# Kernel tuning notes

Hardware: AMD Instinct MI355X
Metric: run time of the kernel (lower is better)

Reference implementation:

```python
import jax, jax.numpy as jnp
import numpy as np

# Synthetic kinematic tree: 1 root + C0 chains of L0 atoms (generation 0 scans,
# rooted at node 0) + C1 branches of L1 atoms rooted mid-chain (generation 1 scans).
C0, L0 = 2048, 768
C1, L1 = 2048, 256
N = 1 + C0 * L0 + C1 * L1  # 2_097_153 atoms (incl. virtual root)


def setup_inputs() -> dict:
    key = jax.random.key(0)
    dofs = jax.random.normal(key, (N, 9), dtype=jnp.float32)

    chain_starts = 1 + np.arange(C0, dtype=np.int64) * L0          # first atom of each chain
    gen0 = np.concatenate(
        [np.zeros((C0, 1), np.int64),
         chain_starts[:, None] + np.arange(L0)[None, :]], axis=1)    # [C0, L0+1], col0 = root

    branch_roots = chain_starts + L0 // 2                            # computed during gen 0
    boff = 1 + C0 * L0
    gen1 = np.concatenate(
        [branch_roots[:, None],
         boff + (np.arange(C1, dtype=np.int64) * L1)[:, None] + np.arange(L1)[None, :]],
        axis=1)                                                      # [C1, L1+1]

    doftype = np.full((N,), 2, np.int32)  # BOND
    doftype[0] = 0                        # ROOT
    doftype[chain_starts] = 1             # JUMP at each chain start

    # kintree.id[1:] -> coords index: a fixed permutation (irregular scatter)
    id_idx = np.random.default_rng(0).permutation(N - 1).astype(np.int32)

    return {
        "dofs": dofs,
        "doftype": jnp.asarray(doftype),
        "gen0_paths": jnp.asarray(gen0, dtype=jnp.int32),
        "gen1_paths": jnp.asarray(gen1, dtype=jnp.int32),
        "id_idx": jnp.asarray(id_idx),
    }


def _rx(a):
    c, s = jnp.cos(a), jnp.sin(a)
    o, z = jnp.ones_like(a), jnp.zeros_like(a)
    return jnp.stack([jnp.stack([o, z, z, z], -1),
                      jnp.stack([z, c, -s, z], -1),
                      jnp.stack([z, s, c, z], -1),
                      jnp.stack([z, z, z, o], -1)], -2)


def _ry(a):
    c, s = jnp.cos(a), jnp.sin(a)
    o, z = jnp.ones_like(a), jnp.zeros_like(a)
    return jnp.stack([jnp.stack([c, z, s, z], -1),
                      jnp.stack([z, o, z, z], -1),
                      jnp.stack([-s, z, c, z], -1),
                      jnp.stack([z, z, z, o], -1)], -2)


def _rz(a):
    c, s = jnp.cos(a), jnp.sin(a)
    o, z = jnp.ones_like(a), jnp.zeros_like(a)
    return jnp.stack([jnp.stack([c, -s, z, z], -1),
                      jnp.stack([s, c, z, z], -1),
                      jnp.stack([z, z, o, z], -1),
                      jnp.stack([z, z, z, o], -1)], -2)


def _trans(x, y, z):
    o, zr = jnp.ones_like(x), jnp.zeros_like(x)
    return jnp.stack([jnp.stack([o, zr, zr, x], -1),
                      jnp.stack([zr, o, zr, y], -1),
                      jnp.stack([zr, zr, o, z], -1),
                      jnp.stack([zr, zr, zr, o], -1)], -2)


def _local_hts(dofs, doftype):
    # BOND dofs: phi_p, theta, d, phi_c  (NeRF-style internal coordinates)
    phi_p, theta, d, phi_c = dofs[:, 0], dofs[:, 1], dofs[:, 2], dofs[:, 3]
    z = jnp.zeros_like(d)
    bond = _rx(phi_p) @ _rz(jnp.pi - theta) @ _trans(d, z, z) @ _rx(phi_c)
    # JUMP dofs: RBx,RBy,RBz, RBdel_(a,b,c), RB_(a,b,c)
    rot = lambda a, b, c: _rz(c) @ _ry(b) @ _rx(a)
    jump = (_trans(dofs[:, 0], dofs[:, 1], dofs[:, 2])
            @ rot(dofs[:, 3], dofs[:, 4], dofs[:, 5])
            @ rot(dofs[:, 6], dofs[:, 7], dofs[:, 8]))
    eye = jnp.broadcast_to(jnp.eye(4, dtype=dofs.dtype), bond.shape)
    dt = doftype[:, None, None]
    return jnp.where(dt == 1, jump, jnp.where(dt == 2, bond, eye))


def reference(dofs, doftype, gen0_paths, gen1_paths, id_idx):
    hts = _local_hts(dofs, doftype)  # [N, 4, 4] local HTs; root = identity
    # Generation-ordered segmented scan: within each generation, each scan path's
    # first node already holds its GLOBAL HT; compose child = parent @ local along
    # the path via an associative prefix-matmul, then scatter back.
    for paths in (gen0_paths, gen1_paths):
        seg = hts[paths]                                        # [S, Lp, 4, 4]
        scanned = jax.lax.associative_scan(jnp.matmul, seg, axis=1)
        hts = hts.at[paths].set(scanned)
    kincoords = hts[:, :3, 3]                                   # [N, 3]
    coords = jnp.zeros((N - 1, 3), dtype=dofs.dtype)
    coords = coords.at[id_idx].set(kincoords[1:])               # coords[id[1:]] = kincoords[1:]
    return coords
```

## Files before the change

### kernel.cpp

```cpp
#include <hip/hip_runtime.h>
#include <math.h>

#define NC0 2048
#define NL0 768
#define NL1 256
#define BOFF (1 + NC0 * NL0)

struct Aff { float f[12]; };

__device__ __forceinline__ Aff affIdentity() {
    Aff M;
    M.f[0]=1.f; M.f[1]=0.f; M.f[2]=0.f;
    M.f[3]=0.f; M.f[4]=1.f; M.f[5]=0.f;
    M.f[6]=0.f; M.f[7]=0.f; M.f[8]=1.f;
    M.f[9]=0.f; M.f[10]=0.f; M.f[11]=0.f;
    return M;
}

__device__ __forceinline__ Aff compose(const Aff& A, const Aff& B) {
    Aff C;
#pragma unroll
    for (int i = 0; i < 3; ++i) {
        const float a0 = A.f[i*3+0], a1 = A.f[i*3+1], a2 = A.f[i*3+2];
#pragma unroll
        for (int j = 0; j < 3; ++j)
            C.f[i*3+j] = a0*B.f[0*3+j] + a1*B.f[1*3+j] + a2*B.f[2*3+j];
        C.f[9+i] = a0*B.f[9] + a1*B.f[10] + a2*B.f[11] + A.f[9+i];
    }
    return C;
}

__device__ __forceinline__ void applyA(const Aff& A, float& x, float& y, float& z) {
    const float nx = A.f[0]*x + A.f[1]*y + A.f[2]*z + A.f[9];
    const float ny = A.f[3]*x + A.f[4]*y + A.f[5]*z + A.f[10];
    const float nz = A.f[6]*x + A.f[7]*y + A.f[8]*z + A.f[11];
    x = nx; y = ny; z = nz;
}

__device__ __forceinline__ Aff shflUpA(const Aff& A, int d) {
    Aff B;
#pragma unroll
    for (int k = 0; k < 12; ++k) B.f[k] = __shfl_up(A.f[k], d, 64);
    return B;
}

__device__ __forceinline__ void fsc(float a, float& s, float& c) {
    s = __sinf(a);
    c = __cosf(a);
}

__device__ __forceinline__ Aff bondHT(float phi_p, float theta, float dd, float phi_c) {
    float sp, cp, st, ct, sc, cc;
    fsc(phi_p, sp, cp);
    fsc(theta, st, ct);
    fsc(phi_c, sc, cc);
    const float ca = -ct, sa = st;
    const float r00 = ca,    r01 = -sa;
    const float r10 = cp*sa, r11 = cp*ca,  r12 = -sp;
    const float r20 = sp*sa, r21 = sp*ca,  r22 = cp;
    Aff M;
    M.f[0] = r00; M.f[1] = r01*cc;          M.f[2] = -r01*sc;
    M.f[3] = r10; M.f[4] = r11*cc + r12*sc; M.f[5] = -r11*sc + r12*cc;
    M.f[6] = r20; M.f[7] = r21*cc + r22*sc; M.f[8] = -r21*sc + r22*cc;
    M.f[9] = r00*dd; M.f[10] = r10*dd; M.f[11] = r20*dd;
    return M;
}

__device__ __forceinline__ void rot3(float a, float b, float c, float* R) {
    float sa, ca, sb, cb, sg, cg;
    fsc(a, sa, ca);
    fsc(b, sb, cb);
    fsc(c, sg, cg);
    R[0] = cb*cg; R[1] = sa*sb*cg - ca*sg; R[2] = ca*sb*cg + sa*sg;
    R[3] = cb*sg; R[4] = sa*sb*sg + ca*cg; R[5] = ca*sb*sg - sa*cg;
    R[6] = -sb;   R[7] = sa*cb;            R[8] = ca*cb;
}

__device__ __forceinline__ Aff jumpHT(float d0, float d1, float d2,
                                      float d3, float d4, float d5,
                                      float d6, float d7, float d8) {
    float R1[9], R2[9];
    rot3(d3, d4, d5, R1);
    rot3(d6, d7, d8, R2);
    Aff M;
#pragma unroll
    for (int i = 0; i < 3; ++i)
#pragma unroll
        for (int j = 0; j < 3; ++j)
            M.f[i*3+j] = R1[i*3+0]*R2[0*3+j] + R1[i*3+1]*R2[1*3+j] + R1[i*3+2]*R2[2*3+j];
    M.f[9] = d0; M.f[10] = d1; M.f[11] = d2;
    return M;
}

__device__ __forceinline__ void stA(float* sm, int i, const Aff& A) {
    float* p = sm + i * 12;
#pragma unroll
    for (int k = 0; k < 12; ++k) p[k] = A.f[k];
}
__device__ __forceinline__ Aff ldA(const float* sm, int i) {
    const float* p = sm + i * 12;
    Aff A;
#pragma unroll
    for (int k = 0; k < 12; ++k) A.f[k] = p[k];
    return A;
}

__global__ __launch_bounds__(256, 4)
void kin_kernel(const float* __restrict__ dofs,
                const int* __restrict__ id_idx,
                float* __restrict__ out) {
    __shared__ float wt0[4 * 12];
    __shared__ float wt1[4 * 12];
    __shared__ float rootSm[12];

    const int c    = blockIdx.x;
    const int t    = threadIdx.x;
    const int lane = t & 63;
    const int wave = t >> 6;

    const int pos = 3 * t;
    const int n0  = 1 + c * NL0 + pos;
    const float* db  = dofs + (size_t)n0 * 9;
    const float* dbb = dofs + (size_t)(BOFF + c * NL1 + t) * 9;

    const float a0 = db[0],  a1 = db[1],  a2 = db[2],  a3 = db[3];
    const float b0 = db[9],  b1 = db[10], b2 = db[11], b3 = db[12];
    const float c0 = db[18], c1 = db[19], c2 = db[20], c3 = db[21];
    const float e0 = dbb[0], e1 = dbb[1], e2 = dbb[2], e3 = dbb[3];

    const int obase = c * NL0 + pos;
    const int oi0 = id_idx[obase + 0];
    const int oi1 = id_idx[obase + 1];
    const int oi2 = id_idx[obase + 2];
    const int oib = id_idx[(BOFF - 1) + c * NL1 + t];

    Aff P1;
    if (t == 0) {
        const float j4 = db[4], j5 = db[5], j6 = db[6], j7 = db[7], j8 = db[8];
        P1 = jumpHT(a0, a1, a2, a3, j4, j5, j6, j7, j8);
    } else {
        P1 = bondHT(a0, a1, a2, a3);
    }
    const Aff P2 = compose(P1, bondHT(b0, b1, b2, b3));
    const Aff P3 = compose(P2, bondHT(c0, c1, c2, c3));
    Aff Sb = bondHT(e0, e1, e2, e3);

    Aff S = P3;
#pragma unroll
    for (int s = 1; s < 64; s <<= 1) {
        const Aff A = shflUpA(S, s);
        const Aff B = shflUpA(Sb, s);
        if (lane >= s) {
            S  = compose(A, S);
            Sb = compose(B, Sb);
        }
    }
    if (lane == 63) { stA(wt0, wave, S); stA(wt1, wave, Sb); }
    __syncthreads();

    Aff E = shflUpA(S, 1);
    Aff EW;
    if (wave == 0) {
        if (lane == 0) E = affIdentity();
        EW = E;
    } else {
        Aff W = ldA(wt0, 0);
        for (int w = 1; w < wave; ++w) W = compose(W, ldA(wt0, w));
        EW = (lane == 0) ? W : compose(W, E);
    }

    float x0 = P1.f[9], y0 = P1.f[10], z0 = P1.f[11]; applyA(EW, x0, y0, z0);
    float x1 = P2.f[9], y1 = P2.f[10], z1 = P2.f[11]; applyA(EW, x1, y1, z1);
    float x2 = P3.f[9], y2 = P3.f[10], z2 = P3.f[11]; applyA(EW, x2, y2, z2);

    if (t == 128) {
        const Aff G = compose(EW, P1);
        stA(rootSm, 0, G);
    }

    float vx = Sb.f[9], vy = Sb.f[10], vz = Sb.f[11];
    for (int w = wave - 1; w >= 0; --w) {
        const Aff Wb = ldA(wt1, w);
        applyA(Wb, vx, vy, vz);
    }
    __syncthreads();

    const Aff R = ldA(rootSm, 0);
    applyA(R, vx, vy, vz);

    float* o;
    o = out + (size_t)oi0 * 3; o[0] = x0; o[1] = y0; o[2] = z0;
    o = out + (size_t)oi1 * 3; o[0] = x1; o[1] = y1; o[2] = z1;
    o = out + (size_t)oi2 * 3; o[0] = x2; o[1] = y2; o[2] = z2;
    o = out + (size_t)oib * 3; o[0] = vx; o[1] = vy; o[2] = vz;
}

extern "C" void kernel_launch(void* const* d_in, const int* in_sizes, int n_in,
                              void* d_out, int out_size, void* d_ws, size_t ws_size,
                              hipStream_t stream) {
    const float* dofs   = (const float*)d_in[0];
    const int*   id_idx = (const int*)d_in[4];
    float*       out    = (float*)d_out;

    hipLaunchKernelGGL(kin_kernel, dim3(NC0), dim3(256), 0, stream,
                       dofs, id_idx, out);
}
```

Before: 163.1 us.

## Use one wave per chain with 12 atoms per thread and vectorized loads

```diff
diff --git a/kernel.cpp b/kernel.cpp
--- a/kernel.cpp
+++ b/kernel.cpp
@@ -28,13 +28,6 @@
         C.f[9+i] = a0*B.f[9] + a1*B.f[10] + a2*B.f[11] + A.f[9+i];
     }
     return C;
-}
-
-__device__ __forceinline__ void applyA(const Aff& A, float& x, float& y, float& z) {
-    const float nx = A.f[0]*x + A.f[1]*y + A.f[2]*z + A.f[9];
-    const float ny = A.f[3]*x + A.f[4]*y + A.f[5]*z + A.f[10];
-    const float nz = A.f[6]*x + A.f[7]*y + A.f[8]*z + A.f[11];
-    x = nx; y = ny; z = nz;
 }
 
 __device__ __forceinline__ Aff shflUpA(const Aff& A, int d) {
@@ -92,107 +85,117 @@
     return M;
 }
 
-__device__ __forceinline__ void stA(float* sm, int i, const Aff& A) {
-    float* p = sm + i * 12;
-#pragma unroll
-    for (int k = 0; k < 12; ++k) p[k] = A.f[k];
-}
-__device__ __forceinline__ Aff ldA(const float* sm, int i) {
-    const float* p = sm + i * 12;
-    Aff A;
-#pragma unroll
-    for (int k = 0; k < 12; ++k) A.f[k] = p[k];
-    return A;
-}
-
-__global__ __launch_bounds__(256, 4)
+__device__ __forceinline__ float f4c(const float4 v, int j) {
+    return j == 0 ? v.x : j == 1 ? v.y : j == 2 ? v.z : v.w;
+}
+__device__ __forceinline__ int i4c(const int4 v, int j) {
+    return j == 0 ? v.x : j == 1 ? v.y : j == 2 ? v.z : v.w;
+}
+
+#define GFA(m) f4c(ch[((m)+1)>>2], ((m)+1)&3)
+#define GFB(m) f4c(chb[((m)+1)>>2], ((m)+1)&3)
+
+__global__ __launch_bounds__(64)
 void kin_kernel(const float* __restrict__ dofs,
                 const int* __restrict__ id_idx,
                 float* __restrict__ out) {
-    __shared__ float wt0[4 * 12];
-    __shared__ float wt1[4 * 12];
-    __shared__ float rootSm[12];
-
-    const int c    = blockIdx.x;
-    const int t    = threadIdx.x;
-    const int lane = t & 63;
-    const int wave = t >> 6;
-
-    const int pos = 3 * t;
-    const int n0  = 1 + c * NL0 + pos;
-    const float* db  = dofs + (size_t)n0 * 9;
-    const float* dbb = dofs + (size_t)(BOFF + c * NL1 + t) * 9;
-
-    const float a0 = db[0],  a1 = db[1],  a2 = db[2],  a3 = db[3];
-    const float b0 = db[9],  b1 = db[10], b2 = db[11], b3 = db[12];
-    const float c0 = db[18], c1 = db[19], c2 = db[20], c3 = db[21];
-    const float e0 = dbb[0], e1 = dbb[1], e2 = dbb[2], e3 = dbb[3];
-
-    const int obase = c * NL0 + pos;
-    const int oi0 = id_idx[obase + 0];
-    const int oi1 = id_idx[obase + 1];
-    const int oi2 = id_idx[obase + 2];
-    const int oib = id_idx[(BOFF - 1) + c * NL1 + t];
-
-    Aff P1;
-    if (t == 0) {
-        const float j4 = db[4], j5 = db[5], j6 = db[6], j7 = db[7], j8 = db[8];
-        P1 = jumpHT(a0, a1, a2, a3, j4, j5, j6, j7, j8);
-    } else {
-        P1 = bondHT(a0, a1, a2, a3);
-    }
-    const Aff P2 = compose(P1, bondHT(b0, b1, b2, b3));
-    const Aff P3 = compose(P2, bondHT(c0, c1, c2, c3));
-    Aff Sb = bondHT(e0, e1, e2, e3);
-
-    Aff S = P3;
+    const int c = blockIdx.x;
+    const int t = threadIdx.x;
+
+    const int ib0 = c * NL0 + 12 * t;
+    const int4 i0 = *(const int4*)(id_idx + ib0 + 0);
+    const int4 i1 = *(const int4*)(id_idx + ib0 + 4);
+    const int4 i2 = *(const int4*)(id_idx + ib0 + 8);
+    const int4 ibv = *(const int4*)(id_idx + (BOFF - 1) + c * NL1 + 4 * t);
+
+    const float4* g4 = (const float4*)dofs;
+    const size_t f0  = (size_t)(1 + c * NL0 + 12 * t) * 9;
+    const size_t cb0 = (f0 - 1) >> 2;
+    float4 ch[26];
+    ch[0]  = g4[cb0 + 0];  ch[1]  = g4[cb0 + 1];  ch[2]  = g4[cb0 + 2];
+    ch[3]  = g4[cb0 + 3];  ch[4]  = g4[cb0 + 4];  ch[5]  = g4[cb0 + 5];
+    ch[7]  = g4[cb0 + 7];  ch[9]  = g4[cb0 + 9];  ch[10] = g4[cb0 + 10];
+    ch[11] = g4[cb0 + 11]; ch[12] = g4[cb0 + 12]; ch[13] = g4[cb0 + 13];
+    ch[14] = g4[cb0 + 14]; ch[16] = g4[cb0 + 16]; ch[18] = g4[cb0 + 18];
+    ch[19] = g4[cb0 + 19]; ch[20] = g4[cb0 + 20]; ch[21] = g4[cb0 + 21];
+    ch[22] = g4[cb0 + 22]; ch[23] = g4[cb0 + 23]; ch[25] = g4[cb0 + 25];
+
+    const size_t f1  = (size_t)(BOFF + c * NL1 + 4 * t) * 9;
+    const size_t cb1 = (f1 - 1) >> 2;
+    float4 chb[8];
+    chb[0] = g4[cb1 + 0]; chb[1] = g4[cb1 + 1]; chb[2] = g4[cb1 + 2];
+    chb[3] = g4[cb1 + 3]; chb[4] = g4[cb1 + 4]; chb[5] = g4[cb1 + 5];
+    chb[7] = g4[cb1 + 7];
+
+    float qx[12], qy[12], qz[12];
+    Aff Q, H0f;
+#pragma unroll
+    for (int k = 0; k < 12; ++k) {
+        Aff H;
+        if (k == 0) {
+            if (t == 0)
+                H = jumpHT(GFA(0), GFA(1), GFA(2), GFA(3), GFA(4),
+                           GFA(5), GFA(6), GFA(7), GFA(8));
+            else
+                H = bondHT(GFA(0), GFA(1), GFA(2), GFA(3));
+            H0f = H;
+            Q = H;
+        } else {
+            H = bondHT(GFA(9*k+0), GFA(9*k+1), GFA(9*k+2), GFA(9*k+3));
+            Q = compose(Q, H);
+        }
+        qx[k] = Q.f[9]; qy[k] = Q.f[10]; qz[k] = Q.f[11];
+    }
+
+    Aff S = Q;
 #pragma unroll
     for (int s = 1; s < 64; s <<= 1) {
-        const Aff A = shflUpA(S, s);
-        const Aff B = shflUpA(Sb, s);
-        if (lane >= s) {
-            S  = compose(A, S);
-            Sb = compose(B, Sb);
-        }
-    }
-    if (lane == 63) { stA(wt0, wave, S); stA(wt1, wave, Sb); }
-    __syncthreads();
-
+        const Aff P = shflUpA(S, s);
+        if (t >= s) S = compose(P, S);
+    }
     Aff E = shflUpA(S, 1);
-    Aff EW;
-    if (wave == 0) {
-        if (lane == 0) E = affIdentity();
-        EW = E;
-    } else {
-        Aff W = ldA(wt0, 0);
-        for (int w = 1; w < wave; ++w) W = compose(W, ldA(wt0, w));
-        EW = (lane == 0) ? W : compose(W, E);
-    }
-
-    float x0 = P1.f[9], y0 = P1.f[10], z0 = P1.f[11]; applyA(EW, x0, y0, z0);
-    float x1 = P2.f[9], y1 = P2.f[10], z1 = P2.f[11]; applyA(EW, x1, y1, z1);
-    float x2 = P3.f[9], y2 = P3.f[10], z2 = P3.f[11]; applyA(EW, x2, y2, z2);
-
-    if (t == 128) {
-        const Aff G = compose(EW, P1);
-        stA(rootSm, 0, G);
-    }
-
-    float vx = Sb.f[9], vy = Sb.f[10], vz = Sb.f[11];
-    for (int w = wave - 1; w >= 0; --w) {
-        const Aff Wb = ldA(wt1, w);
-        applyA(Wb, vx, vy, vz);
-    }
-    __syncthreads();
-
-    const Aff R = ldA(rootSm, 0);
-    applyA(R, vx, vy, vz);
-
-    float* o;
-    o = out + (size_t)oi0 * 3; o[0] = x0; o[1] = y0; o[2] = z0;
-    o = out + (size_t)oi1 * 3; o[0] = x1; o[1] = y1; o[2] = z1;
-    o = out + (size_t)oi2 * 3; o[0] = x2; o[1] = y2; o[2] = z2;
-    o = out + (size_t)oib * 3; o[0] = vx; o[1] = vy; o[2] = vz;
+    if (t == 0) E = affIdentity();
+
+#pragma unroll
+    for (int k = 0; k < 12; ++k) {
+        const int oi = (k < 4) ? i4c(i0, k) : (k < 8) ? i4c(i1, k - 4) : i4c(i2, k - 8);
+        float* o = out + (size_t)oi * 3;
+        o[0] = E.f[0]*qx[k] + E.f[1]*qy[k] + E.f[2]*qz[k] + E.f[9];
+        o[1] = E.f[3]*qx[k] + E.f[4]*qy[k] + E.f[5]*qz[k] + E.f[10];
+        o[2] = E.f[6]*qx[k] + E.f[7]*qy[k] + E.f[8]*qz[k] + E.f[11];
+    }
+
+    Aff G = compose(E, H0f);
+#pragma unroll
+    for (int j = 0; j < 12; ++j) G.f[j] = __shfl(G.f[j], 32, 64);
+
+    float rx[4], ry[4], rz[4];
+    Aff R;
+#pragma unroll
+    for (int k = 0; k < 4; ++k) {
+        const Aff Hb = bondHT(GFB(9*k+0), GFB(9*k+1), GFB(9*k+2), GFB(9*k+3));
+        R = (k == 0) ? Hb : compose(R, Hb);
+        rx[k] = R.f[9]; ry[k] = R.f[10]; rz[k] = R.f[11];
+    }
+
+    Aff Sb = R;
+#pragma unroll
+    for (int s = 1; s < 64; s <<= 1) {
+        const Aff P = shflUpA(Sb, s);
+        if (t >= s) Sb = compose(P, Sb);
+    }
+    Aff E1 = shflUpA(Sb, 1);
+    if (t == 0) E1 = affIdentity();
+
+    const Aff M = compose(G, E1);
+#pragma unroll
+    for (int k = 0; k < 4; ++k) {
+        const int oi = i4c(ibv, k);
+        float* o = out + (size_t)oi * 3;
+        o[0] = M.f[0]*rx[k] + M.f[1]*ry[k] + M.f[2]*rz[k] + M.f[9];
+        o[1] = M.f[3]*rx[k] + M.f[4]*ry[k] + M.f[5]*rz[k] + M.f[10];
+        o[2] = M.f[6]*rx[k] + M.f[7]*ry[k] + M.f[8]*rz[k] + M.f[11];
+    }
 }
 
 extern "C" void kernel_launch(void* const* d_in, const int* in_sizes, int n_in,
@@ -202,6 +205,6 @@
     const int*   id_idx = (const int*)d_in[4];
     float*       out    = (float*)d_out;
 
-    hipLaunchKernelGGL(kin_kernel, dim3(NC0), dim3(256), 0, stream,
+    hipLaunchKernelGGL(kin_kernel, dim3(NC0), dim3(64), 0, stream,
                        dofs, id_idx, out);
 }
```

Result: no change. 163.5 us (+0.2%).
